# Performance work log

Hardware: AMD Instinct MI355X
Metric: run time of the kernel (lower is better)

Reference implementation:

```python
import jax, jax.numpy as jnp
import numpy as np


def _pairwise_sqdist(x, y):
    # x: [B, N, 3], y: [B, M, 3] -> [B, N, M] squared distances
    x2 = jnp.sum(x * x, axis=-1, keepdims=True)          # [B, N, 1]
    y2 = jnp.sum(y * y, axis=-1)[:, None, :]             # [B, 1, M]
    xy = jnp.einsum('bnd,bmd->bnm', x, y)                # [B, N, M]
    return jnp.maximum(x2 + y2 - 2.0 * xy, 0.0)


def _chamfer_l1(x, y):
    # PoinTr-style ChamferDistanceL1: mean sqrt NN dist both ways, averaged
    d = _pairwise_sqdist(x, y)                           # [B, N, M]
    d1 = jnp.sqrt(jnp.min(d, axis=2))                    # x -> nearest in y
    d2 = jnp.sqrt(jnp.min(d, axis=1))                    # y -> nearest in x
    return 0.5 * (jnp.mean(d1) + jnp.mean(d2))


def setup_inputs() -> dict:
    key = jax.random.key(0)
    k1, k2, k3, k4 = jax.random.split(key, 4)
    B, Nc, Nf = 4, 1024, 8192
    return {
        'ret_coarse': jax.random.normal(k1, (B, Nc, 3), dtype=jnp.float32),
        'ret_fine':   jax.random.normal(k2, (B, Nf, 3), dtype=jnp.float32),
        'gt_fine':    jax.random.normal(k3, (B, Nf, 3), dtype=jnp.float32),
        'gt_coarse':  jax.random.normal(k4, (B, Nc, 3), dtype=jnp.float32),
    }


def reference(ret_coarse, ret_fine, gt_fine, gt_coarse):
    loss_fine = _chamfer_l1(ret_fine, gt_fine)
    # coarse L2 point-distance loss: mean over (B, Nc) of per-point L2 norm
    loss_coarse = jnp.mean(jnp.sqrt(jnp.sum((ret_coarse - gt_coarse) ** 2, axis=2)))
    return (loss_coarse, loss_fine)
```

## Files before the change

### kernel.cpp

```cpp
#include <hip/hip_runtime.h>

#define B  4
#define NF 8192
#define NC 1024
#define TJ (NF / 32)
#define BANDS 128
#define TPW 32

#define NMIN (2 * B * NF)
#define NCRS (B * NC)
#define NTOT (NMIN + NCRS)

typedef _Float16 h8   __attribute__((ext_vector_type(8)));
typedef float    f16v __attribute__((ext_vector_type(16)));


__global__ __launch_bounds__(256) void k_prep(const float* __restrict__ rf,
                                              const float* __restrict__ gf,
                                              h8* __restrict__ fragbuf) {
    int id  = blockIdx.x * 256 + threadIdx.x;
    int src = id >> 16;
    int rem = id & 65535;
    int b   = rem >> 14;
    int jt  = (rem >> 6) & (TJ - 1);
    int ln  = rem & 63;
    int n   = ln & 31, kg = ln >> 5;

    const float* y = (src ? rf : gf) + ((size_t)(b * NF) + jt * 32 + n) * 3;
    float y0 = y[0], y1 = y[1], y2 = y[2];
    float t0 = -2.0f * y0, t1 = -2.0f * y1, t2 = -2.0f * y2;
    _Float16 mh0 = (_Float16)t0, mh1 = (_Float16)t1, mh2 = (_Float16)t2;
    _Float16 ml0 = (_Float16)(t0 - (float)mh0);
    _Float16 ml1 = (_Float16)(t1 - (float)mh1);
    _Float16 ml2 = (_Float16)(t2 - (float)mh2);
    float sy = fmaf(y0, y0, fmaf(y1, y1, y2 * y2));
    _Float16 syh = (_Float16)sy;
    _Float16 syl = (_Float16)(sy - (float)syh);

    h8 fr = {};
    if (kg == 0) {
        fr[0] = mh0; fr[1] = mh1; fr[2] = mh2;
        fr[3] = mh0; fr[4] = mh1; fr[5] = mh2;
        fr[6] = ml0; fr[7] = ml1;
    } else {
        fr[0] = ml2; fr[1] = (_Float16)1.0f; fr[2] = (_Float16)1.0f;
        fr[3] = syh; fr[4] = syl;
    }
    fragbuf[((size_t)(src * B + b) * TJ + jt) * 64 + ln] = fr;
}

__global__ __launch_bounds__(512) void k_main(const float* __restrict__ rf,
                                              const float* __restrict__ gf,
                                              const h8* __restrict__ fragbuf,
                                              float* __restrict__ rowbuf) {
    __shared__ float rbuf[8][64];

    int bx   = blockIdx.x;
    int dir  = bx >> 9;
    int rem  = bx & 511;
    int b    = rem >> 7;
    int band = rem & 127;
    int t  = threadIdx.x;
    int ln = t & 63, w = t >> 6, m = ln & 31, kg = ln >> 5;

    const float* xp = dir ? gf : rf;
    h8 afr[2];
#pragma unroll
    for (int f = 0; f < 2; ++f) {
        const float* xr = xp + ((size_t)(b * NF) + band * 64 + f * 32 + m) * 3;
        float x0 = xr[0], x1 = xr[1], x2 = xr[2];
        _Float16 h0 = (_Float16)x0, h1 = (_Float16)x1, h2 = (_Float16)x2;
        _Float16 l0 = (_Float16)(x0 - (float)h0);
        _Float16 l1 = (_Float16)(x1 - (float)h1);
        _Float16 l2 = (_Float16)(x2 - (float)h2);
        float sx = fmaf(x0, x0, fmaf(x1, x1, x2 * x2));
        _Float16 sh = (_Float16)sx;
        _Float16 sl = (_Float16)(sx - (float)sh);
        h8 fr = {};
        if (kg == 0) {
            fr[0] = h0; fr[1] = h1; fr[2] = h2;
            fr[3] = l0; fr[4] = l1; fr[5] = l2;
            fr[6] = h0; fr[7] = h1;
        } else {
            fr[0] = h2; fr[1] = sh; fr[2] = sl;
            fr[3] = (_Float16)1.0f; fr[4] = (_Float16)1.0f;
        }
        afr[f] = fr;
    }

    float rmin0[16], rmin1[16];
#pragma unroll
    for (int r = 0; r < 16; ++r) { rmin0[r] = 3.4e38f; rmin1[r] = 3.4e38f; }

    const h8* p = fragbuf + ((size_t)(dir * B + b) * TJ + w * TPW) * 64 + ln;
    h8 b0 = p[0];
    h8 b1 = p[64];
#pragma unroll 2
    for (int q = 0; q < TPW / 2; ++q) {
        h8 n0 = p[(2 * q + 2) * 64];
        h8 n1 = p[(2 * q + 3) * 64];
        f16v c00 = __builtin_amdgcn_mfma_f32_32x32x16_f16(afr[0], b0, (f16v){}, 0, 0, 0);
        f16v c01 = __builtin_amdgcn_mfma_f32_32x32x16_f16(afr[0], b1, (f16v){}, 0, 0, 0);
#pragma unroll
        for (int r = 0; r < 16; ++r)
            rmin0[r] = fminf(fminf(c00[r], c01[r]), rmin0[r]);
        f16v c10 = __builtin_amdgcn_mfma_f32_32x32x16_f16(afr[1], b0, (f16v){}, 0, 0, 0);
        f16v c11 = __builtin_amdgcn_mfma_f32_32x32x16_f16(afr[1], b1, (f16v){}, 0, 0, 0);
#pragma unroll
        for (int r = 0; r < 16; ++r)
            rmin1[r] = fminf(fminf(c10[r], c11[r]), rmin1[r]);
        b0 = n0;
        b1 = n1;
    }

#pragma unroll
    for (int off = 1; off <= 16; off <<= 1) {
#pragma unroll
        for (int r = 0; r < 16; ++r) {
            rmin0[r] = fminf(rmin0[r], __shfl_xor(rmin0[r], off));
            rmin1[r] = fminf(rmin1[r], __shfl_xor(rmin1[r], off));
        }
    }
    if (m == 0) {
#pragma unroll
        for (int r = 0; r < 16; ++r) {
            int row = 4 * kg + (r & 3) + 8 * (r >> 2);
            rbuf[w][row]      = rmin0[r];
            rbuf[w][32 + row] = rmin1[r];
        }
    }
    __syncthreads();
    if (t < 64) {
        float v = rbuf[0][t];
#pragma unroll
        for (int ww = 1; ww < 8; ++ww) v = fminf(v, rbuf[ww][t]);
        rowbuf[(size_t)dir * (B * NF) + b * NF + band * 64 + t] =
            sqrtf(fmaxf(v, 0.0f));
    }
}

__global__ __launch_bounds__(256) void k_reduce(const float* __restrict__ rowbuf,
                                                const float* __restrict__ rc,
                                                const float* __restrict__ gc,
                                                float* __restrict__ out) {
    float s_crs = 0.f, s_fine = 0.f;
    for (int i = blockIdx.x * 256 + threadIdx.x; i < NTOT; i += gridDim.x * 256) {
        if (i < NMIN) {
            s_fine += rowbuf[i];
        } else {
            int pnt = i - NMIN;
            float dx = rc[3 * pnt + 0] - gc[3 * pnt + 0];
            float dy = rc[3 * pnt + 1] - gc[3 * pnt + 1];
            float dz = rc[3 * pnt + 2] - gc[3 * pnt + 2];
            s_crs += sqrtf(fmaf(dx, dx, fmaf(dy, dy, dz * dz)));
        }
    }
#pragma unroll
    for (int off = 32; off > 0; off >>= 1) {
        s_crs  += __shfl_down(s_crs, off);
        s_fine += __shfl_down(s_fine, off);
    }
    __shared__ float red[2][4];
    int lane = threadIdx.x & 63, w = threadIdx.x >> 6;
    if (lane == 0) { red[0][w] = s_crs; red[1][w] = s_fine; }
    __syncthreads();
    if (threadIdx.x == 0) {
        float t0 = red[0][0] + red[0][1] + red[0][2] + red[0][3];
        float t1 = red[1][0] + red[1][1] + red[1][2] + red[1][3];
        atomicAdd(&out[0], t0 * (1.0f / (float)NCRS));
        atomicAdd(&out[1], t1 * (0.5f / (float)(B * NF)));
    }
}

extern "C" void kernel_launch(void* const* d_in, const int* in_sizes, int n_in,
                              void* d_out, int out_size, void* d_ws, size_t ws_size,
                              hipStream_t stream) {
    const float* rc = (const float*)d_in[0];
    const float* rf = (const float*)d_in[1];
    const float* gf = (const float*)d_in[2];
    const float* gc = (const float*)d_in[3];

    float* rowbuf  = (float*)d_ws;
    h8*    fragbuf = (h8*)((char*)d_ws + (size_t)NMIN * 4);
    float* out     = (float*)d_out;

    hipMemsetAsync(out, 0, 2 * sizeof(float), stream);
    k_prep<<<512, 256, 0, stream>>>(rf, gf, fragbuf);
    k_main<<<2 * B * BANDS, 512, 0, stream>>>(rf, gf, fragbuf, rowbuf);
    k_reduce<<<64, 256, 0, stream>>>(rowbuf, rc, gc, out);
}
```

Before: 95.24 us.

## Fuse final reduction into main kernel and coarse loss into prep kernel

```diff
diff --git a/kernel.cpp b/kernel.cpp
--- a/kernel.cpp
+++ b/kernel.cpp
@@ -6,10 +6,7 @@
 #define TJ (NF / 32)
 #define BANDS 128
 #define TPW 32
-
-#define NMIN (2 * B * NF)
 #define NCRS (B * NC)
-#define NTOT (NMIN + NCRS)
 
 typedef _Float16 h8   __attribute__((ext_vector_type(8)));
 typedef float    f16v __attribute__((ext_vector_type(16)));
@@ -17,7 +14,32 @@
 
 __global__ __launch_bounds__(256) void k_prep(const float* __restrict__ rf,
                                               const float* __restrict__ gf,
-                                              h8* __restrict__ fragbuf) {
+                                              const float* __restrict__ rc,
+                                              const float* __restrict__ gc,
+                                              h8* __restrict__ fragbuf,
+                                              float* __restrict__ out) {
+    if (blockIdx.x == 512) {
+        int t = threadIdx.x;
+        float s = 0.0f;
+        for (int i = t; i < NCRS; i += 256) {
+            float dx = rc[3 * i + 0] - gc[3 * i + 0];
+            float dy = rc[3 * i + 1] - gc[3 * i + 1];
+            float dz = rc[3 * i + 2] - gc[3 * i + 2];
+            s += sqrtf(fmaf(dx, dx, fmaf(dy, dy, dz * dz)));
+        }
+#pragma unroll
+        for (int off = 32; off > 0; off >>= 1) s += __shfl_down(s, off);
+        __shared__ float red[4];
+        int lane = t & 63, w = t >> 6;
+        if (lane == 0) red[w] = s;
+        __syncthreads();
+        if (t == 0) {
+            out[0] = (red[0] + red[1] + red[2] + red[3]) * (1.0f / (float)NCRS);
+            out[1] = 0.0f;
+        }
+        return;
+    }
+
     int id  = blockIdx.x * 256 + threadIdx.x;
     int src = id >> 16;
     int rem = id & 65535;
@@ -52,7 +74,7 @@
 __global__ __launch_bounds__(512) void k_main(const float* __restrict__ rf,
                                               const float* __restrict__ gf,
                                               const h8* __restrict__ fragbuf,
-                                              float* __restrict__ rowbuf) {
+                                              float* __restrict__ out) {
     __shared__ float rbuf[8][64];
 
     int bx   = blockIdx.x;
@@ -134,41 +156,10 @@
         float v = rbuf[0][t];
 #pragma unroll
         for (int ww = 1; ww < 8; ++ww) v = fminf(v, rbuf[ww][t]);
-        rowbuf[(size_t)dir * (B * NF) + b * NF + band * 64 + t] =
-            sqrtf(fmaxf(v, 0.0f));
-    }
-}
-
-__global__ __launch_bounds__(256) void k_reduce(const float* __restrict__ rowbuf,
-                                                const float* __restrict__ rc,
-                                                const float* __restrict__ gc,
-                                                float* __restrict__ out) {
-    float s_crs = 0.f, s_fine = 0.f;
-    for (int i = blockIdx.x * 256 + threadIdx.x; i < NTOT; i += gridDim.x * 256) {
-        if (i < NMIN) {
-            s_fine += rowbuf[i];
-        } else {
-            int pnt = i - NMIN;
-            float dx = rc[3 * pnt + 0] - gc[3 * pnt + 0];
-            float dy = rc[3 * pnt + 1] - gc[3 * pnt + 1];
-            float dz = rc[3 * pnt + 2] - gc[3 * pnt + 2];
-            s_crs += sqrtf(fmaf(dx, dx, fmaf(dy, dy, dz * dz)));
-        }
-    }
+        v = sqrtf(fmaxf(v, 0.0f));
 #pragma unroll
-    for (int off = 32; off > 0; off >>= 1) {
-        s_crs  += __shfl_down(s_crs, off);
-        s_fine += __shfl_down(s_fine, off);
-    }
-    __shared__ float red[2][4];
-    int lane = threadIdx.x & 63, w = threadIdx.x >> 6;
-    if (lane == 0) { red[0][w] = s_crs; red[1][w] = s_fine; }
-    __syncthreads();
-    if (threadIdx.x == 0) {
-        float t0 = red[0][0] + red[0][1] + red[0][2] + red[0][3];
-        float t1 = red[1][0] + red[1][1] + red[1][2] + red[1][3];
-        atomicAdd(&out[0], t0 * (1.0f / (float)NCRS));
-        atomicAdd(&out[1], t1 * (0.5f / (float)(B * NF)));
+        for (int off = 32; off > 0; off >>= 1) v += __shfl_down(v, off);
+        if (t == 0) atomicAdd(&out[1], v * (0.5f / (float)(B * NF)));
     }
 }
 
@@ -180,12 +171,9 @@
     const float* gf = (const float*)d_in[2];
     const float* gc = (const float*)d_in[3];
 
-    float* rowbuf  = (float*)d_ws;
-    h8*    fragbuf = (h8*)((char*)d_ws + (size_t)NMIN * 4);
+    h8*    fragbuf = (h8*)d_ws;
     float* out     = (float*)d_out;
 
-    hipMemsetAsync(out, 0, 2 * sizeof(float), stream);
-    k_prep<<<512, 256, 0, stream>>>(rf, gf, fragbuf);
-    k_main<<<2 * B * BANDS, 512, 0, stream>>>(rf, gf, fragbuf, rowbuf);
-    k_reduce<<<64, 256, 0, stream>>>(rowbuf, rc, gc, out);
+    k_prep<<<513, 256, 0, stream>>>(rf, gf, rc, gc, fragbuf, out);
+    k_main<<<2 * B * BANDS, 512, 0, stream>>>(rf, gf, fragbuf, out);
 }
```

After: 99.62 us. +4.6%, slower.
